# Kernel optimization log

Hardware: AMD Instinct MI355X
Metric: run time of the kernel (lower is better)

## Reference

```python
import jax, jax.numpy as jnp
import numpy as np

N, IN_DIM, OUT_DIM = 8192, 128, 128

def setup_inputs() -> dict:
    key = jax.random.key(0)
    k1, k2, k3, k4 = jax.random.split(key, 4)
    X = jax.random.normal(k1, (N, IN_DIM), dtype=jnp.float32)
    A = jax.random.uniform(k2, (N, N), dtype=jnp.float32)
    # nn.Linear(in_dim, out_dim): W [out,in], b [out]
    bound = 1.0 / np.sqrt(IN_DIM)
    W = jax.random.uniform(k3, (OUT_DIM, IN_DIM), minval=-bound, maxval=bound, dtype=jnp.float32)
    b = jax.random.uniform(k4, (OUT_DIM,), minval=-bound, maxval=bound, dtype=jnp.float32)
    return {"X": X, "A": A, "W": W, "b": b}

def reference(X, A, W, b):
    n = A.shape[0]
    A_hat = A + jnp.eye(n, dtype=A.dtype)                 # A + I
    d_inv_sqrt = A_hat.sum(axis=1) ** -0.5                # [N]
    # D^-1/2 @ A_hat @ D^-1/2 == row/col scaling (same math, no diag GEMMs)
    A_norm = d_inv_sqrt[:, None] * A_hat * d_inv_sqrt[None, :]
    H = A_norm @ X                                        # [N, in_dim]
    return H @ W.T + b                                    # [N, out_dim]
```

## Files before the change

### kernel.cpp

```cpp
#include <hip/hip_runtime.h>

#define N_NODES 8192
#define DIM 128

typedef short bf16x8 __attribute__((ext_vector_type(8)));
typedef float f32x4 __attribute__((ext_vector_type(4)));

__device__ __forceinline__ unsigned short f2bf_rne(float x) {
    unsigned int u = __builtin_bit_cast(unsigned int, x);
    u += 0x7fffu + ((u >> 16) & 1u);
    return (unsigned short)(u >> 16);
}
__device__ __forceinline__ float bf2f(unsigned short h) {
    unsigned int u = ((unsigned int)h) << 16;
    return __builtin_bit_cast(float, u);
}

__global__ __launch_bounds__(256) void k_rowsum(const float* __restrict__ A,
                                                float* __restrict__ d) {
    int row = blockIdx.x;
    const float4* Ar = (const float4*)(A + (size_t)row * N_NODES);
    int t = threadIdx.x;
    float s = 0.f;
#pragma unroll
    for (int i = 0; i < 8; ++i) {
        float4 v = Ar[t + i * 256];
        s += (v.x + v.y) + (v.z + v.w);
    }
#pragma unroll
    for (int off = 32; off > 0; off >>= 1)
        s += __shfl_down(s, off, 64);
    __shared__ float wsum[4];
    if ((t & 63) == 0) wsum[t >> 6] = s;
    __syncthreads();
    if (t == 0) {
        float tot = wsum[0] + wsum[1] + wsum[2] + wsum[3] + 1.0f;
        d[row] = rsqrtf(tot);
    }
}

__global__ __launch_bounds__(256) void k_zgemm(const float* __restrict__ X,
                                               const float* __restrict__ W,
                                               const float* __restrict__ d,
                                               unsigned short* __restrict__ Zt) {
    __shared__ float Xs[64][129];
    __shared__ float Ws[64][129];
    int rb = blockIdx.x >> 1;
    int cb = blockIdx.x & 1;
    int t = threadIdx.x;
    const float4* Xg = (const float4*)(X + (size_t)rb * 64 * DIM);
    const float4* Wg = (const float4*)(W + (size_t)cb * 64 * DIM);
#pragma unroll
    for (int i = 0; i < 8; ++i) {
        int f = t + i * 256;
        int r = f >> 5;
        int c = (f & 31) << 2;
        float4 v = Xg[f];
        Xs[r][c] = v.x; Xs[r][c + 1] = v.y; Xs[r][c + 2] = v.z; Xs[r][c + 3] = v.w;
        float4 w = Wg[f];
        Ws[r][c] = w.x; Ws[r][c + 1] = w.y; Ws[r][c + 2] = w.z; Ws[r][c + 3] = w.w;
    }
    __syncthreads();
    int tx = t & 15, ty = t >> 4;
    float acc[4][4] = {};
    for (int k = 0; k < DIM; ++k) {
        float xr[4], wr[4];
#pragma unroll
        for (int i = 0; i < 4; ++i) xr[i] = Xs[ty * 4 + i][k];
#pragma unroll
        for (int j = 0; j < 4; ++j) wr[j] = Ws[tx * 4 + j][k];
#pragma unroll
        for (int i = 0; i < 4; ++i)
#pragma unroll
            for (int j = 0; j < 4; ++j)
                acc[i][j] += xr[i] * wr[j];
    }
#pragma unroll
    for (int i = 0; i < 4; ++i) {
        int row = rb * 64 + ty * 4 + i;
        float dv = d[row];
#pragma unroll
        for (int j = 0; j < 4; ++j) {
            int col = cb * 64 + tx * 4 + j;
            Zt[(size_t)col * N_NODES + row] = f2bf_rne(dv * acc[i][j]);
        }
    }
}

__global__ __launch_bounds__(64) void k_spmm(const float* __restrict__ A,
                                             const unsigned short* __restrict__ Zt,
                                             const float* __restrict__ d,
                                             const float* __restrict__ bias,
                                             float* __restrict__ out) {
    int lane = threadIdx.x;
    int l15 = lane & 15, quad = lane >> 4;
    int row0 = blockIdx.x * 16;

    const float* Arow = A + (size_t)(row0 + l15) * N_NODES + quad * 8;
    const unsigned short* Zb = Zt + (size_t)l15 * N_NODES + quad * 8;

    f32x4 acc[8];
#pragma unroll
    for (int i = 0; i < 8; ++i) acc[i] = (f32x4){0.f, 0.f, 0.f, 0.f};

    for (int k = 0; k < N_NODES; k += 32) {
        f32x4 a0 = *(const f32x4*)(Arow + k);
        f32x4 a1 = *((const f32x4*)(Arow + k) + 1);
        bf16x8 af;
        af[0] = (short)f2bf_rne(a0[0]); af[1] = (short)f2bf_rne(a0[1]);
        af[2] = (short)f2bf_rne(a0[2]); af[3] = (short)f2bf_rne(a0[3]);
        af[4] = (short)f2bf_rne(a1[0]); af[5] = (short)f2bf_rne(a1[1]);
        af[6] = (short)f2bf_rne(a1[2]); af[7] = (short)f2bf_rne(a1[3]);
        bf16x8 bfr[8];
#pragma unroll
        for (int n = 0; n < 8; ++n)
            bfr[n] = *(const bf16x8*)(Zb + (size_t)n * 16 * N_NODES + k);
#pragma unroll
        for (int n = 0; n < 8; ++n)
            acc[n] = __builtin_amdgcn_mfma_f32_16x16x32_bf16(af, bfr[n], acc[n], 0, 0, 0);
    }

#pragma unroll
    for (int n = 0; n < 8; ++n) {
        int col = n * 16 + l15;
        float bcol = bias[col];
#pragma unroll
        for (int r = 0; r < 4; ++r) {
            int row = row0 + quad * 4 + r;
            float zid = bf2f(Zt[(size_t)col * N_NODES + row]);
            out[(size_t)row * DIM + col] = d[row] * (acc[n][r] + zid) + bcol;
        }
    }
}

extern "C" void kernel_launch(void* const* d_in, const int* in_sizes, int n_in,
                              void* d_out, int out_size, void* d_ws, size_t ws_size,
                              hipStream_t stream) {
    const float* X = (const float*)d_in[0];
    const float* A = (const float*)d_in[1];
    const float* W = (const float*)d_in[2];
    const float* b = (const float*)d_in[3];
    float* out = (float*)d_out;

    char* ws = (char*)d_ws;
    float* dinv = (float*)ws;
    unsigned short* Zt = (unsigned short*)(ws + 32768);

    k_rowsum<<<N_NODES, 256, 0, stream>>>(A, dinv);
    k_zgemm<<<256, 256, 0, stream>>>(X, W, dinv, Zt);
    k_spmm<<<512, 64, 0, stream>>>(A, Zt, dinv, b, out);
}
```

Measured before the change: 522.4 us.

## Split SpMM K dimension across four waves with partial-sum reduction kernel

The dense A·Z GEMM kernel now launches 256-thread blocks, and each of the four wavefronts handles a quarter of the K range for the same 16-row tile. This gives four times more waves in flight to hide the memory latency of streaming A. Partial results are written to a workspace buffer. A new reduce kernel sums them and applies the degree scaling and bias. The cost is an extra 16 MB of partial-sum traffic plus one more kernel launch.

```diff
diff --git a/kernel.cpp b/kernel.cpp
--- a/kernel.cpp
+++ b/kernel.cpp
@@ -87,12 +87,12 @@
     }
 }
 
-__global__ __launch_bounds__(64) void k_spmm(const float* __restrict__ A,
-                                             const unsigned short* __restrict__ Zt,
-                                             const float* __restrict__ d,
-                                             const float* __restrict__ bias,
-                                             float* __restrict__ out) {
-    int lane = threadIdx.x;
+__global__ __launch_bounds__(256) void k_spmm(const float* __restrict__ A,
+                                              const unsigned short* __restrict__ Zt,
+                                              float* __restrict__ part) {
+    int t = threadIdx.x;
+    int w = t >> 6;
+    int lane = t & 63;
     int l15 = lane & 15, quad = lane >> 4;
     int row0 = blockIdx.x * 16;
 
@@ -103,7 +103,8 @@
 #pragma unroll
     for (int i = 0; i < 8; ++i) acc[i] = (f32x4){0.f, 0.f, 0.f, 0.f};
 
-    for (int k = 0; k < N_NODES; k += 32) {
+    int kbeg = w * (N_NODES / 4);
+    for (int k = kbeg; k < kbeg + N_NODES / 4; k += 32) {
         f32x4 a0 = *(const f32x4*)(Arow + k);
         f32x4 a1 = *((const f32x4*)(Arow + k) + 1);
         bf16x8 af;
@@ -120,17 +121,37 @@
             acc[n] = __builtin_amdgcn_mfma_f32_16x16x32_bf16(af, bfr[n], acc[n], 0, 0, 0);
     }
 
+    float* pw = part + (size_t)w * N_NODES * DIM;
 #pragma unroll
     for (int n = 0; n < 8; ++n) {
         int col = n * 16 + l15;
-        float bcol = bias[col];
 #pragma unroll
         for (int r = 0; r < 4; ++r) {
             int row = row0 + quad * 4 + r;
-            float zid = bf2f(Zt[(size_t)col * N_NODES + row]);
-            out[(size_t)row * DIM + col] = d[row] * (acc[n][r] + zid) + bcol;
+            float v = acc[n][r];
+            if (w == 0) v += bf2f(Zt[(size_t)col * N_NODES + row]);
+            pw[(size_t)row * DIM + col] = v;
         }
     }
+}
+
+__global__ __launch_bounds__(256) void k_reduce(const float* __restrict__ part,
+                                                const float* __restrict__ d,
+                                                const float* __restrict__ bias,
+                                                float* __restrict__ out) {
+    int f = (blockIdx.x * 256 + threadIdx.x) * 4;
+    int row = f >> 7;
+    int c0 = f & 127;
+    const size_t S = (size_t)N_NODES * DIM;
+    f32x4 p0 = *(const f32x4*)(part + f);
+    f32x4 p1 = *(const f32x4*)(part + S + f);
+    f32x4 p2 = *(const f32x4*)(part + 2 * S + f);
+    f32x4 p3 = *(const f32x4*)(part + 3 * S + f);
+    f32x4 bb = *(const f32x4*)(bias + c0);
+    float dv = d[row];
+    f32x4 o = (p0 + p1) + (p2 + p3);
+    o = o * dv + bb;
+    *(f32x4*)(out + f) = o;
 }
 
 extern "C" void kernel_launch(void* const* d_in, const int* in_sizes, int n_in,
@@ -145,8 +166,10 @@
     char* ws = (char*)d_ws;
     float* dinv = (float*)ws;
     unsigned short* Zt = (unsigned short*)(ws + 32768);
+    float* part = (float*)(ws + 32768 + 2 * 1024 * 1024);
 
     k_rowsum<<<N_NODES, 256, 0, stream>>>(A, dinv);
     k_zgemm<<<256, 256, 0, stream>>>(X, W, dinv, Zt);
-    k_spmm<<<512, 64, 0, stream>>>(A, Zt, dinv, b, out);
+    k_spmm<<<512, 256, 0, stream>>>(A, Zt, part);
+    k_reduce<<<N_NODES * DIM / 4 / 256, 256, 0, stream>>>(part, dinv, b, out);
 }
```

New measurement: 531.0 us. No clear change (+1.7%).
